# Kernel optimization log

Measured on AMD Instinct MI355X. Metric: run time of the kernel, lower is better.

Reference implementation:

```python
import jax, jax.numpy as jnp
import numpy as np

N_NODES = 50000
N_EDGES = 600000
D = 128
EDGE_VOCAB = 10


def setup_inputs() -> dict:
    key = jax.random.key(0)
    ks = jax.random.split(key, 8)
    x = jax.random.normal(ks[0], (N_NODES, D), dtype=jnp.float32)
    edge_index = jax.random.randint(ks[1], (2, N_EDGES), 0, N_NODES, dtype=jnp.int64)
    edge_weight = jax.random.randint(ks[2], (N_EDGES,), 0, EDGE_VOCAB, dtype=jnp.int64)
    cat_list = jax.random.randint(ks[3], (N_NODES,), 0, 4, dtype=jnp.int64)
    # edge embedding initialized uniform [0,1) as in torch.nn.init.uniform_
    edge_emb = jax.random.uniform(ks[4], (EDGE_VOCAB, D), dtype=jnp.float32)
    # nn.Linear default init ~ U(-1/sqrt(in), 1/sqrt(in))
    lim = 1.0 / np.sqrt(D)
    W_l = jax.random.uniform(ks[5], (D, D), minval=-lim, maxval=lim, dtype=jnp.float32)
    b_l = jax.random.uniform(ks[6], (D,), minval=-lim, maxval=lim, dtype=jnp.float32)
    W_r = jax.random.uniform(ks[7], (D, D), minval=-lim, maxval=lim, dtype=jnp.float32)
    b_r = jax.random.uniform(jax.random.fold_in(key, 99), (D,), minval=-lim, maxval=lim, dtype=jnp.float32)
    return {"x": x, "edge_emb": edge_emb, "W_l": W_l, "b_l": b_l,
            "W_r": W_r, "b_r": b_r, "edge_index": edge_index,
            "edge_weight": edge_weight, "cat_list": cat_list}


def reference(x, edge_emb, W_l, b_l, W_r, b_r, edge_index, edge_weight, cat_list):
    # Active H_GAT path: real_GNN(x, edge_index, edge_weight)
    src = edge_index[0]  # x_j (source nodes, PyG source_to_target flow)
    dst = edge_index[1]  # aggregation index
    # message: edge embedding lookup * gathered neighbor features  [E, D]
    msg = edge_emb[edge_weight] * x[src]
    # aggregate: scatter-sum to destination nodes  [N, D]
    prop = jax.ops.segment_sum(msg, dst, num_segments=x.shape[0])
    # out = lin_l(x) + lin_r(prop)
    out = x @ W_l.T + b_l + prop @ W_r.T + b_r
    return out
```

## Files before the change

kernel.cpp:

```cpp
#include <hip/hip_runtime.h>

#define N_NODES 50000
#define N_EDGES 600000
#define D 128
#define SCAN_BLOCKS ((N_NODES + 255) / 256)
#define PACK_CAP 1351680
#define PFILL_BLOCKS (PACK_CAP / 1024)
#define SENTINEL 50000u

typedef __attribute__((ext_vector_type(8))) short short8v;
typedef __attribute__((ext_vector_type(4))) float f32x4;

__device__ __forceinline__ unsigned short f2bf(float v) {
    unsigned u = __builtin_bit_cast(unsigned, v);
    u += 0x7FFFu + ((u >> 16) & 1u);
    return (unsigned short)(u >> 16);
}
__device__ __forceinline__ float bf2f(unsigned short h) {
    unsigned u = ((unsigned)h) << 16;
    return __builtin_bit_cast(float, u);
}

#define XPREP_BLOCKS ((N_NODES * D / 8 + 255) / 256)
__global__ __launch_bounds__(256) void prep_kernel(
    const float* __restrict__ Wl, const float* __restrict__ Wr,
    unsigned short* __restrict__ Bh, unsigned short* __restrict__ Bl,
    const float* __restrict__ x, unsigned short* __restrict__ xbf,
    int* __restrict__ counts, unsigned* __restrict__ packed)
{
    int bid = blockIdx.x;
    if (bid < 128) {
        int t = bid * 256 + threadIdx.x;
        int n = t >> 8;
        int k = t & 255;
        float w = (k < 128) ? Wl[n * 128 + k] : Wr[n * 128 + (k - 128)];
        unsigned short h = f2bf(w);
        Bh[t] = h;
        Bl[t] = f2bf(w - bf2f(h));
    } else if (bid < 128 + XPREP_BLOCKS) {
        int t = (bid - 128) * 256 + threadIdx.x;
        if (t < N_NODES * D / 8) {
            const float4* p = (const float4*)(x + (size_t)t * 8);
            float4 a = p[0], b = p[1];
            short8v o;
            o[0] = (short)f2bf(a.x); o[1] = (short)f2bf(a.y);
            o[2] = (short)f2bf(a.z); o[3] = (short)f2bf(a.w);
            o[4] = (short)f2bf(b.x); o[5] = (short)f2bf(b.y);
            o[6] = (short)f2bf(b.z); o[7] = (short)f2bf(b.w);
            *(short8v*)(xbf + (size_t)t * 8) = o;
        }
    } else if (bid < 128 + XPREP_BLOCKS + SCAN_BLOCKS) {
        int t = (bid - 128 - XPREP_BLOCKS) * 256 + threadIdx.x;
        if (t < N_NODES) counts[t] = 0;
    } else if (bid < 128 + XPREP_BLOCKS + SCAN_BLOCKS + PFILL_BLOCKS) {
        int t = (bid - 128 - XPREP_BLOCKS - SCAN_BLOCKS) * 1024 + threadIdx.x * 4;
        uint4 s = make_uint4(SENTINEL, SENTINEL, SENTINEL, SENTINEL);
        *(uint4*)(packed + t) = s;
    } else {
        if (threadIdx.x < 16) {
            short8v z = (short8v){0,0,0,0,0,0,0,0};
            *(short8v*)(xbf + (size_t)N_NODES * D + threadIdx.x * 8) = z;
        }
    }
}


__global__ __launch_bounds__(256) void histrank_kernel(
    const int* __restrict__ ei, int* __restrict__ counts,
    int* __restrict__ rank)
{
    int e = blockIdx.x * blockDim.x + threadIdx.x;
    if (e >= N_EDGES) return;
    rank[e] = atomicAdd(&counts[ei[N_EDGES + e]], 1);
}

__global__ __launch_bounds__(256) void scan_phase1(
    const int* __restrict__ counts, int* __restrict__ blockSums)
{
    int i = blockIdx.x * 256 + threadIdx.x;
    int v = (i < N_NODES) ? ((counts[i] + 15) & ~15) : 0;
#pragma unroll
    for (int off = 32; off > 0; off >>= 1) v += __shfl_down(v, off, 64);
    __shared__ int wsum[4];
    int lane = threadIdx.x & 63, wid = threadIdx.x >> 6;
    if (lane == 0) wsum[wid] = v;
    __syncthreads();
    if (threadIdx.x == 0)
        blockSums[blockIdx.x] = wsum[0] + wsum[1] + wsum[2] + wsum[3];
}

__global__ __launch_bounds__(256) void scan_phase2(
    const int* __restrict__ blockSums, int* __restrict__ blockOffs,
    int* __restrict__ offs)
{
    __shared__ int sh[256];
    int t = threadIdx.x;
    int v = (t < SCAN_BLOCKS) ? blockSums[t] : 0;
    sh[t] = v;
    __syncthreads();
    for (int off = 1; off < 256; off <<= 1) {
        int u = (t >= off) ? sh[t - off] : 0;
        __syncthreads();
        sh[t] += u;
        __syncthreads();
    }
    if (t < SCAN_BLOCKS) blockOffs[t] = sh[t] - v;
    if (t == 255) offs[N_NODES] = sh[255];
}

__global__ __launch_bounds__(256) void scan_phase3(
    const int* __restrict__ counts,
    const int* __restrict__ blockOffs,
    int* __restrict__ offs)
{
    int t = threadIdx.x;
    int i = blockIdx.x * 256 + t;
    int v = (i < N_NODES) ? ((counts[i] + 15) & ~15) : 0;
    int lane = t & 63, wid = t >> 6;
    int s = v;
#pragma unroll
    for (int off = 1; off < 64; off <<= 1) {
        int u = __shfl_up(s, off, 64);
        if (lane >= off) s += u;
    }
    __shared__ int wsum[4];
    if (lane == 63) wsum[wid] = s;
    __syncthreads();
    int wadd = 0;
    for (int w = 0; w < wid; w++) wadd += wsum[w];
    if (i < N_NODES)
        offs[i] = blockOffs[blockIdx.x] + s + wadd - v;
}

__global__ __launch_bounds__(256) void pack_kernel(
    const int* __restrict__ ei,
    const int* __restrict__ ew,
    const int* __restrict__ offs,
    const int* __restrict__ rank,
    unsigned* __restrict__ packed)
{
    int e = blockIdx.x * blockDim.x + threadIdx.x;
    if (e >= N_EDGES) return;
    int dst = ei[N_EDGES + e];
    int r   = rank[e];
    int pos = offs[dst] + r;
    packed[pos] = (unsigned)ei[e] | ((unsigned)ew[e] << 16);
}

__global__ __launch_bounds__(256) void aggregate_kernel(
    const unsigned short* __restrict__ xbf,
    const float* __restrict__ emb,
    const int* __restrict__ offs,
    const unsigned* __restrict__ packed,
    float* __restrict__ prop)
{
    __shared__ float emb_s[10][D];
    for (int i = threadIdx.x; i < 10 * D; i += 256)
        emb_s[i >> 7][i & 127] = emb[i];
    __syncthreads();

    int node = blockIdx.x * 8 + (threadIdx.x >> 5);
    if (node >= N_NODES) return;
    int c = (threadIdx.x & 31) * 4;

    int beg = offs[node], end = offs[node + 1];
    float4 acc = make_float4(0.f, 0.f, 0.f, 0.f);

    for (int i = beg; __any(i < end); i += 16) {
        int ib = (i < end) ? i : (PACK_CAP - 16);
        uint4 pk4[4];
#pragma unroll
        for (int qq = 0; qq < 4; qq++)
            pk4[qq] = *(const uint4*)(packed + ib + qq * 4);
        unsigned pk[16];
#pragma unroll
        for (int qq = 0; qq < 4; qq++) {
            pk[qq*4+0] = pk4[qq].x; pk[qq*4+1] = pk4[qq].y;
            pk[qq*4+2] = pk4[qq].z; pk[qq*4+3] = pk4[qq].w;
        }
        uint2 xr[16];
#pragma unroll
        for (int q = 0; q < 16; q++)
            xr[q] = *(const uint2*)(xbf + (size_t)(pk[q] & 0xFFFFu) * D + c);
#pragma unroll
        for (int q = 0; q < 16; q++) {
            float4 er = *(const float4*)&emb_s[pk[q] >> 16][c];
            acc.x += er.x * bf2f((unsigned short)(xr[q].x & 0xFFFFu));
            acc.y += er.y * bf2f((unsigned short)(xr[q].x >> 16));
            acc.z += er.z * bf2f((unsigned short)(xr[q].y & 0xFFFFu));
            acc.w += er.w * bf2f((unsigned short)(xr[q].y >> 16));
        }
    }
    *(float4*)(prop + (size_t)node * D + c) = acc;
}


__global__ void zero_kernel(float4* __restrict__ out, int n4) {
    int i = blockIdx.x * blockDim.x + threadIdx.x;
    int stride = gridDim.x * blockDim.x;
    for (; i < n4; i += stride) out[i] = make_float4(0.f, 0.f, 0.f, 0.f);
}

__global__ __launch_bounds__(256) void scatter_kernel(
    const float* __restrict__ x,
    const float* __restrict__ emb,
    const int*   __restrict__ ei,
    const int*   __restrict__ ew,
    float*       __restrict__ prop)
{
    int gid = blockIdx.x * blockDim.x + threadIdx.x;
    int e = gid >> 5;
    if (e >= N_EDGES) return;
    int d4 = (gid & 31) * 4;
    int src = ei[e];
    int dst = ei[N_EDGES + e];
    int w   = ew[e];
    float4 ev = *(const float4*)(emb + (size_t)w * D + d4);
    float4 xv = *(const float4*)(x + (size_t)src * D + d4);
    float* p = prop + (size_t)dst * D + d4;
    atomicAdd(p + 0, ev.x * xv.x);
    atomicAdd(p + 1, ev.y * xv.y);
    atomicAdd(p + 2, ev.z * xv.z);
    atomicAdd(p + 3, ev.w * xv.w);
}


__global__ __launch_bounds__(256) void mfma_gemm(
    const float* __restrict__ x,
    float*       __restrict__ out,
    const unsigned short* __restrict__ Bh,
    const unsigned short* __restrict__ Bl,
    const float* __restrict__ bl_,
    const float* __restrict__ br_)
{
    __shared__ unsigned short Ah_s[128 * 40];
    __shared__ unsigned short Al_s[128 * 40];
    __shared__ unsigned short Bh_s[128 * 40];
    __shared__ unsigned short Bl_s[128 * 40];

    const int tid  = threadIdx.x;
    const int lane = tid & 63;
    const int wave = tid >> 6;
    const int row0 = blockIdx.x * 128;

    const int wr0 = (wave >> 1) * 64;
    const int wc0 = (wave & 1) * 64;
    const int lr  = lane & 15;
    const int lk8 = (lane >> 4) * 8;

    const int srow  = tid >> 1;
    const int skoff = (tid & 1) * 16;

    f32x4 acc[4][4];
#pragma unroll
    for (int i = 0; i < 4; i++)
#pragma unroll
        for (int j = 0; j < 4; j++)
            acc[i][j] = (f32x4){0.f, 0.f, 0.f, 0.f};

    for (int kc = 0; kc < 8; ++kc) {
        const int kbase = kc * 32;
        {
            const float* Asrc = (kbase < 128) ? x : out;
            const int acol = (kbase & 127) + skoff;
            const int grow = row0 + srow;
            float v[16];
            if (grow < N_NODES) {
                const float4* p = (const float4*)(Asrc + (size_t)grow * D + acol);
#pragma unroll
                for (int q = 0; q < 4; q++) {
                    float4 f = p[q];
                    v[q*4+0] = f.x; v[q*4+1] = f.y; v[q*4+2] = f.z; v[q*4+3] = f.w;
                }
            } else {
#pragma unroll
                for (int q = 0; q < 16; q++) v[q] = 0.f;
            }
            short8v h0, h1, l0, l1;
#pragma unroll
            for (int q = 0; q < 8; q++) {
                unsigned short h = f2bf(v[q]);
                h0[q] = (short)h;
                l0[q] = (short)f2bf(v[q] - bf2f(h));
            }
#pragma unroll
            for (int q = 0; q < 8; q++) {
                unsigned short h = f2bf(v[q + 8]);
                h1[q] = (short)h;
                l1[q] = (short)f2bf(v[q + 8] - bf2f(h));
            }
            *(short8v*)(Ah_s + srow * 40 + skoff)     = h0;
            *(short8v*)(Ah_s + srow * 40 + skoff + 8) = h1;
            *(short8v*)(Al_s + srow * 40 + skoff)     = l0;
            *(short8v*)(Al_s + srow * 40 + skoff + 8) = l1;
        }
        {
            const size_t boff = (size_t)srow * 256 + kbase + skoff;
            short8v bh0 = *(const short8v*)(Bh + boff);
            short8v bh1 = *(const short8v*)(Bh + boff + 8);
            short8v bl0 = *(const short8v*)(Bl + boff);
            short8v bl1 = *(const short8v*)(Bl + boff + 8);
            *(short8v*)(Bh_s + srow * 40 + skoff)     = bh0;
            *(short8v*)(Bh_s + srow * 40 + skoff + 8) = bh1;
            *(short8v*)(Bl_s + srow * 40 + skoff)     = bl0;
            *(short8v*)(Bl_s + srow * 40 + skoff + 8) = bl1;
        }
        __syncthreads();
        short8v afh[4], afl[4];
#pragma unroll
        for (int rt = 0; rt < 4; rt++) {
            int ar = wr0 + rt * 16 + lr;
            afh[rt] = *(const short8v*)(Ah_s + ar * 40 + lk8);
            afl[rt] = *(const short8v*)(Al_s + ar * 40 + lk8);
        }
#pragma unroll
        for (int ct = 0; ct < 4; ct++) {
            int bc = wc0 + ct * 16 + lr;
            short8v bfh = *(const short8v*)(Bh_s + bc * 40 + lk8);
            short8v bfl = *(const short8v*)(Bl_s + bc * 40 + lk8);
#pragma unroll
            for (int rt = 0; rt < 4; rt++)
                acc[rt][ct] = __builtin_amdgcn_mfma_f32_16x16x32_bf16(afh[rt], bfh, acc[rt][ct], 0, 0, 0);
#pragma unroll
            for (int rt = 0; rt < 4; rt++)
                acc[rt][ct] = __builtin_amdgcn_mfma_f32_16x16x32_bf16(afl[rt], bfh, acc[rt][ct], 0, 0, 0);
#pragma unroll
            for (int rt = 0; rt < 4; rt++)
                acc[rt][ct] = __builtin_amdgcn_mfma_f32_16x16x32_bf16(afh[rt], bfl, acc[rt][ct], 0, 0, 0);
        }
        __syncthreads();
    }

    const int drow = (lane >> 4) * 4;
#pragma unroll
    for (int ct = 0; ct < 4; ct++) {
        int col = wc0 + ct * 16 + lr;
        float bias = bl_[col] + br_[col];
#pragma unroll
        for (int rt = 0; rt < 4; rt++) {
#pragma unroll
            for (int r = 0; r < 4; r++) {
                int grow = row0 + wr0 + rt * 16 + drow + r;
                if (grow < N_NODES)
                    out[(size_t)grow * D + col] = acc[rt][ct][r] + bias;
            }
        }
    }
}

extern "C" void kernel_launch(void* const* d_in, const int* in_sizes, int n_in,
                              void* d_out, int out_size, void* d_ws, size_t ws_size,
                              hipStream_t stream) {
    const float* x    = (const float*)d_in[0];
    const float* emb  = (const float*)d_in[1];
    const float* W_l  = (const float*)d_in[2];
    const float* b_l  = (const float*)d_in[3];
    const float* W_r  = (const float*)d_in[4];
    const float* b_r  = (const float*)d_in[5];
    const int*   ei   = (const int*)d_in[6];
    const int*   ew   = (const int*)d_in[7];

    float* out = (float*)d_out;

    char* wsp = (char*)d_ws;
    unsigned short* Bh  = (unsigned short*)wsp; wsp += 128 * 256 * sizeof(unsigned short);
    unsigned short* Bl  = (unsigned short*)wsp; wsp += 128 * 256 * sizeof(unsigned short);
    unsigned short* xbf = (unsigned short*)wsp; wsp += (size_t)(N_NODES + 1) * D * sizeof(unsigned short);
    int*      counts    = (int*)wsp;     wsp += N_NODES * sizeof(int);
    int*      offs      = (int*)wsp;     wsp += (N_NODES + 1) * sizeof(int);
    int*      rank      = (int*)wsp;     wsp += N_EDGES * sizeof(int);
    int*      blockSums = (int*)wsp;     wsp += SCAN_BLOCKS * sizeof(int);
    int*      blockOffs = (int*)wsp;     wsp += SCAN_BLOCKS * sizeof(int);
    unsigned* packed    = (unsigned*)wsp; wsp += (size_t)PACK_CAP * sizeof(unsigned);
    size_t needed = (size_t)(wsp - (char*)d_ws);

    if (ws_size >= needed) {
        prep_kernel<<<128 + XPREP_BLOCKS + SCAN_BLOCKS + PFILL_BLOCKS + 1, 256, 0, stream>>>(
            W_l, W_r, Bh, Bl, x, xbf, counts, packed);
        histrank_kernel<<<(N_EDGES + 255) / 256, 256, 0, stream>>>(ei, counts, rank);
        scan_phase1<<<SCAN_BLOCKS, 256, 0, stream>>>(counts, blockSums);
        scan_phase2<<<1, 256, 0, stream>>>(blockSums, blockOffs, offs);
        scan_phase3<<<SCAN_BLOCKS, 256, 0, stream>>>(counts, blockOffs, offs);
        pack_kernel<<<(N_EDGES + 255) / 256, 256, 0, stream>>>(ei, ew, offs, rank, packed);
        aggregate_kernel<<<(N_NODES + 7) / 8, 256, 0, stream>>>(xbf, emb, offs, packed, out);
        mfma_gemm<<<(N_NODES + 127) / 128, 256, 0, stream>>>(x, out, Bh, Bl, b_l, b_r);
    } else {
        prep_kernel<<<128, 256, 0, stream>>>(W_l, W_r, Bh, Bl, x, xbf, counts, packed);
        int n4 = N_NODES * D / 4;
        zero_kernel<<<(n4 + 255) / 256, 256, 0, stream>>>((float4*)out, n4);
        long long work = (long long)N_EDGES * 32;
        scatter_kernel<<<(int)((work + 255) / 256), 256, 0, stream>>>(x, emb, ei, ew, out);
        mfma_gemm<<<(N_NODES + 127) / 128, 256, 0, stream>>>(x, out, Bh, Bl, b_l, b_r);
    }
}
```

Baseline: 106.7 us.

## Pre-split x and prop into bf16 hi/lo, shrink CSR padding, merge scan phases

```diff
diff --git a/kernel.cpp b/kernel.cpp
--- a/kernel.cpp
+++ b/kernel.cpp
@@ -4,7 +4,8 @@
 #define N_EDGES 600000
 #define D 128
 #define SCAN_BLOCKS ((N_NODES + 255) / 256)
-#define PACK_CAP 1351680
+#define PAD 8
+#define PACK_CAP 950272
 #define PFILL_BLOCKS (PACK_CAP / 1024)
 #define SENTINEL 50000u
 
@@ -25,7 +26,8 @@
 __global__ __launch_bounds__(256) void prep_kernel(
     const float* __restrict__ Wl, const float* __restrict__ Wr,
     unsigned short* __restrict__ Bh, unsigned short* __restrict__ Bl,
-    const float* __restrict__ x, unsigned short* __restrict__ xbf,
+    const float* __restrict__ x,
+    unsigned short* __restrict__ xh, unsigned short* __restrict__ xl,
     int* __restrict__ counts, unsigned* __restrict__ packed)
 {
     int bid = blockIdx.x;
@@ -42,12 +44,16 @@
         if (t < N_NODES * D / 8) {
             const float4* p = (const float4*)(x + (size_t)t * 8);
             float4 a = p[0], b = p[1];
-            short8v o;
-            o[0] = (short)f2bf(a.x); o[1] = (short)f2bf(a.y);
-            o[2] = (short)f2bf(a.z); o[3] = (short)f2bf(a.w);
-            o[4] = (short)f2bf(b.x); o[5] = (short)f2bf(b.y);
-            o[6] = (short)f2bf(b.z); o[7] = (short)f2bf(b.w);
-            *(short8v*)(xbf + (size_t)t * 8) = o;
+            float v[8] = {a.x, a.y, a.z, a.w, b.x, b.y, b.z, b.w};
+            short8v oh, ol;
+#pragma unroll
+            for (int q = 0; q < 8; q++) {
+                unsigned short h = f2bf(v[q]);
+                oh[q] = (short)h;
+                ol[q] = (short)f2bf(v[q] - bf2f(h));
+            }
+            *(short8v*)(xh + (size_t)t * 8) = oh;
+            *(short8v*)(xl + (size_t)t * 8) = ol;
         }
     } else if (bid < 128 + XPREP_BLOCKS + SCAN_BLOCKS) {
         int t = (bid - 128 - XPREP_BLOCKS) * 256 + threadIdx.x;
@@ -59,7 +65,7 @@
     } else {
         if (threadIdx.x < 16) {
             short8v z = (short8v){0,0,0,0,0,0,0,0};
-            *(short8v*)(xbf + (size_t)N_NODES * D + threadIdx.x * 8) = z;
+            *(short8v*)(xh + (size_t)N_NODES * D + threadIdx.x * 8) = z;
         }
     }
 }
@@ -78,7 +84,7 @@
     const int* __restrict__ counts, int* __restrict__ blockSums)
 {
     int i = blockIdx.x * 256 + threadIdx.x;
-    int v = (i < N_NODES) ? ((counts[i] + 15) & ~15) : 0;
+    int v = (i < N_NODES) ? ((counts[i] + PAD - 1) & ~(PAD - 1)) : 0;
 #pragma unroll
     for (int off = 32; off > 0; off >>= 1) v += __shfl_down(v, off, 64);
     __shared__ int wsum[4];
@@ -89,14 +95,15 @@
         blockSums[blockIdx.x] = wsum[0] + wsum[1] + wsum[2] + wsum[3];
 }
 
-__global__ __launch_bounds__(256) void scan_phase2(
-    const int* __restrict__ blockSums, int* __restrict__ blockOffs,
+__global__ __launch_bounds__(256) void scan_phase23(
+    const int* __restrict__ counts,
+    const int* __restrict__ blockSums,
     int* __restrict__ offs)
 {
     __shared__ int sh[256];
     int t = threadIdx.x;
-    int v = (t < SCAN_BLOCKS) ? blockSums[t] : 0;
-    sh[t] = v;
+    int bs = (t < SCAN_BLOCKS) ? blockSums[t] : 0;
+    sh[t] = bs;
     __syncthreads();
     for (int off = 1; off < 256; off <<= 1) {
         int u = (t >= off) ? sh[t - off] : 0;
@@ -104,18 +111,11 @@
         sh[t] += u;
         __syncthreads();
     }
-    if (t < SCAN_BLOCKS) blockOffs[t] = sh[t] - v;
-    if (t == 255) offs[N_NODES] = sh[255];
-}
-
-__global__ __launch_bounds__(256) void scan_phase3(
-    const int* __restrict__ counts,
-    const int* __restrict__ blockOffs,
-    int* __restrict__ offs)
-{
-    int t = threadIdx.x;
+    int blockOff = (blockIdx.x > 0) ? sh[blockIdx.x - 1] : 0;
+    if (blockIdx.x == 0 && t == 0) offs[N_NODES] = sh[SCAN_BLOCKS - 1];
+
     int i = blockIdx.x * 256 + t;
-    int v = (i < N_NODES) ? ((counts[i] + 15) & ~15) : 0;
+    int v = (i < N_NODES) ? ((counts[i] + PAD - 1) & ~(PAD - 1)) : 0;
     int lane = t & 63, wid = t >> 6;
     int s = v;
 #pragma unroll
@@ -129,7 +129,7 @@
     int wadd = 0;
     for (int w = 0; w < wid; w++) wadd += wsum[w];
     if (i < N_NODES)
-        offs[i] = blockOffs[blockIdx.x] + s + wadd - v;
+        offs[i] = blockOff + s + wadd - v;
 }
 
 __global__ __launch_bounds__(256) void pack_kernel(
@@ -148,11 +148,11 @@
 }
 
 __global__ __launch_bounds__(256) void aggregate_kernel(
-    const unsigned short* __restrict__ xbf,
+    const unsigned short* __restrict__ xh,
     const float* __restrict__ emb,
     const int* __restrict__ offs,
     const unsigned* __restrict__ packed,
-    float* __restrict__ prop)
+    unsigned short* __restrict__ ph, unsigned short* __restrict__ pl)
 {
     __shared__ float emb_s[10][D];
     for (int i = threadIdx.x; i < 10 * D; i += 256)
@@ -166,24 +166,17 @@
     int beg = offs[node], end = offs[node + 1];
     float4 acc = make_float4(0.f, 0.f, 0.f, 0.f);
 
-    for (int i = beg; __any(i < end); i += 16) {
-        int ib = (i < end) ? i : (PACK_CAP - 16);
-        uint4 pk4[4];
-#pragma unroll
-        for (int qq = 0; qq < 4; qq++)
-            pk4[qq] = *(const uint4*)(packed + ib + qq * 4);
-        unsigned pk[16];
-#pragma unroll
-        for (int qq = 0; qq < 4; qq++) {
-            pk[qq*4+0] = pk4[qq].x; pk[qq*4+1] = pk4[qq].y;
-            pk[qq*4+2] = pk4[qq].z; pk[qq*4+3] = pk4[qq].w;
-        }
-        uint2 xr[16];
-#pragma unroll
-        for (int q = 0; q < 16; q++)
-            xr[q] = *(const uint2*)(xbf + (size_t)(pk[q] & 0xFFFFu) * D + c);
-#pragma unroll
-        for (int q = 0; q < 16; q++) {
+    for (int i = beg; __any(i < end); i += PAD) {
+        int ib = (i < end) ? i : (PACK_CAP - PAD);
+        uint4 a0 = *(const uint4*)(packed + ib);
+        uint4 a1 = *(const uint4*)(packed + ib + 4);
+        unsigned pk[8] = {a0.x, a0.y, a0.z, a0.w, a1.x, a1.y, a1.z, a1.w};
+        uint2 xr[8];
+#pragma unroll
+        for (int q = 0; q < 8; q++)
+            xr[q] = *(const uint2*)(xh + (size_t)(pk[q] & 0xFFFFu) * D + c);
+#pragma unroll
+        for (int q = 0; q < 8; q++) {
             float4 er = *(const float4*)&emb_s[pk[q] >> 16][c];
             acc.x += er.x * bf2f((unsigned short)(xr[q].x & 0xFFFFu));
             acc.y += er.y * bf2f((unsigned short)(xr[q].x >> 16));
@@ -191,7 +184,127 @@
             acc.w += er.w * bf2f((unsigned short)(xr[q].y >> 16));
         }
     }
-    *(float4*)(prop + (size_t)node * D + c) = acc;
+    float v[4] = {acc.x, acc.y, acc.z, acc.w};
+    unsigned short h[4], l[4];
+#pragma unroll
+    for (int q = 0; q < 4; q++) {
+        h[q] = f2bf(v[q]);
+        l[q] = f2bf(v[q] - bf2f(h[q]));
+    }
+    unsigned h01 = (unsigned)h[0] | ((unsigned)h[1] << 16);
+    unsigned h23 = (unsigned)h[2] | ((unsigned)h[3] << 16);
+    unsigned l01 = (unsigned)l[0] | ((unsigned)l[1] << 16);
+    unsigned l23 = (unsigned)l[2] | ((unsigned)l[3] << 16);
+    *(uint2*)(ph + (size_t)node * D + c) = make_uint2(h01, h23);
+    *(uint2*)(pl + (size_t)node * D + c) = make_uint2(l01, l23);
+}
+
+__global__ __launch_bounds__(256) void mfma_gemm(
+    const unsigned short* __restrict__ xh, const unsigned short* __restrict__ xl,
+    const unsigned short* __restrict__ ph, const unsigned short* __restrict__ pl,
+    float*       __restrict__ out,
+    const unsigned short* __restrict__ Bh,
+    const unsigned short* __restrict__ Bl,
+    const float* __restrict__ bl_,
+    const float* __restrict__ br_)
+{
+    __shared__ unsigned short Ah_s[128 * 40];
+    __shared__ unsigned short Al_s[128 * 40];
+    __shared__ unsigned short Bh_s[128 * 40];
+    __shared__ unsigned short Bl_s[128 * 40];
+
+    const int tid  = threadIdx.x;
+    const int lane = tid & 63;
+    const int wave = tid >> 6;
+    const int row0 = blockIdx.x * 128;
+
+    const int wr0 = (wave >> 1) * 64;
+    const int wc0 = (wave & 1) * 64;
+    const int lr  = lane & 15;
+    const int lk8 = (lane >> 4) * 8;
+
+    const int srow  = tid >> 1;
+    const int skoff = (tid & 1) * 16;
+
+    f32x4 acc[4][4];
+#pragma unroll
+    for (int i = 0; i < 4; i++)
+#pragma unroll
+        for (int j = 0; j < 4; j++)
+            acc[i][j] = (f32x4){0.f, 0.f, 0.f, 0.f};
+
+    for (int kc = 0; kc < 8; ++kc) {
+        const int kbase = kc * 32;
+        {
+            const unsigned short* sH = (kbase < 128) ? xh : ph;
+            const unsigned short* sL = (kbase < 128) ? xl : pl;
+            const size_t off = (size_t)(row0 + srow) * D + (kbase & 127) + skoff;
+            short8v h0, h1, l0, l1;
+            if (row0 + srow < N_NODES) {
+                h0 = *(const short8v*)(sH + off);
+                h1 = *(const short8v*)(sH + off + 8);
+                l0 = *(const short8v*)(sL + off);
+                l1 = *(const short8v*)(sL + off + 8);
+            } else {
+                h0 = h1 = l0 = l1 = (short8v){0,0,0,0,0,0,0,0};
+            }
+            *(short8v*)(Ah_s + srow * 40 + skoff)     = h0;
+            *(short8v*)(Ah_s + srow * 40 + skoff + 8) = h1;
+            *(short8v*)(Al_s + srow * 40 + skoff)     = l0;
+            *(short8v*)(Al_s + srow * 40 + skoff + 8) = l1;
+        }
+        {
+            const size_t boff = (size_t)srow * 256 + kbase + skoff;
+            short8v bh0 = *(const short8v*)(Bh + boff);
+            short8v bh1 = *(const short8v*)(Bh + boff + 8);
+            short8v bl0 = *(const short8v*)(Bl + boff);
+            short8v bl1 = *(const short8v*)(Bl + boff + 8);
+            *(short8v*)(Bh_s + srow * 40 + skoff)     = bh0;
+            *(short8v*)(Bh_s + srow * 40 + skoff + 8) = bh1;
+            *(short8v*)(Bl_s + srow * 40 + skoff)     = bl0;
+            *(short8v*)(Bl_s + srow * 40 + skoff + 8) = bl1;
+        }
+        __syncthreads();
+        short8v afh[4], afl[4];
+#pragma unroll
+        for (int rt = 0; rt < 4; rt++) {
+            int ar = wr0 + rt * 16 + lr;
+            afh[rt] = *(const short8v*)(Ah_s + ar * 40 + lk8);
+            afl[rt] = *(const short8v*)(Al_s + ar * 40 + lk8);
+        }
+#pragma unroll
+        for (int ct = 0; ct < 4; ct++) {
+            int bc = wc0 + ct * 16 + lr;
+            short8v bfh = *(const short8v*)(Bh_s + bc * 40 + lk8);
+            short8v bfl = *(const short8v*)(Bl_s + bc * 40 + lk8);
+#pragma unroll
+            for (int rt = 0; rt < 4; rt++)
+                acc[rt][ct] = __builtin_amdgcn_mfma_f32_16x16x32_bf16(afh[rt], bfh, acc[rt][ct], 0, 0, 0);
+#pragma unroll
+            for (int rt = 0; rt < 4; rt++)
+                acc[rt][ct] = __builtin_amdgcn_mfma_f32_16x16x32_bf16(afl[rt], bfh, acc[rt][ct], 0, 0, 0);
+#pragma unroll
+            for (int rt = 0; rt < 4; rt++)
+                acc[rt][ct] = __builtin_amdgcn_mfma_f32_16x16x32_bf16(afh[rt], bfl, acc[rt][ct], 0, 0, 0);
+        }
+        __syncthreads();
+    }
+
+    const int drow = (lane >> 4) * 4;
+#pragma unroll
+    for (int ct = 0; ct < 4; ct++) {
+        int col = wc0 + ct * 16 + lr;
+        float bias = bl_[col] + br_[col];
+#pragma unroll
+        for (int rt = 0; rt < 4; rt++) {
+#pragma unroll
+            for (int r = 0; r < 4; r++) {
+                int grow = row0 + wr0 + rt * 16 + drow + r;
+                if (grow < N_NODES)
+                    out[(size_t)grow * D + col] = acc[rt][ct][r] + bias;
+            }
+        }
+    }
 }
 
 
@@ -224,8 +337,7 @@
     atomicAdd(p + 3, ev.w * xv.w);
 }
 
-
-__global__ __launch_bounds__(256) void mfma_gemm(
+__global__ __launch_bounds__(256) void mfma_gemm_fb(
     const float* __restrict__ x,
     float*       __restrict__ out,
     const unsigned short* __restrict__ Bh,
@@ -242,12 +354,10 @@
     const int lane = tid & 63;
     const int wave = tid >> 6;
     const int row0 = blockIdx.x * 128;
-
     const int wr0 = (wave >> 1) * 64;
     const int wc0 = (wave & 1) * 64;
     const int lr  = lane & 15;
     const int lk8 = (lane >> 4) * 8;
-
     const int srow  = tid >> 1;
     const int skoff = (tid & 1) * 16;
 
@@ -296,14 +406,10 @@
         }
         {
             const size_t boff = (size_t)srow * 256 + kbase + skoff;
-            short8v bh0 = *(const short8v*)(Bh + boff);
-            short8v bh1 = *(const short8v*)(Bh + boff + 8);
-            short8v bl0 = *(const short8v*)(Bl + boff);
-            short8v bl1 = *(const short8v*)(Bl + boff + 8);
-            *(short8v*)(Bh_s + srow * 40 + skoff)     = bh0;
-            *(short8v*)(Bh_s + srow * 40 + skoff + 8) = bh1;
-            *(short8v*)(Bl_s + srow * 40 + skoff)     = bl0;
-            *(short8v*)(Bl_s + srow * 40 + skoff + 8) = bl1;
+            *(short8v*)(Bh_s + srow * 40 + skoff)     = *(const short8v*)(Bh + boff);
+            *(short8v*)(Bh_s + srow * 40 + skoff + 8) = *(const short8v*)(Bh + boff + 8);
+            *(short8v*)(Bl_s + srow * 40 + skoff)     = *(const short8v*)(Bl + boff);
+            *(short8v*)(Bl_s + srow * 40 + skoff + 8) = *(const short8v*)(Bl + boff + 8);
         }
         __syncthreads();
         short8v afh[4], afl[4];
@@ -365,31 +471,32 @@
     char* wsp = (char*)d_ws;
     unsigned short* Bh  = (unsigned short*)wsp; wsp += 128 * 256 * sizeof(unsigned short);
     unsigned short* Bl  = (unsigned short*)wsp; wsp += 128 * 256 * sizeof(unsigned short);
-    unsigned short* xbf = (unsigned short*)wsp; wsp += (size_t)(N_NODES + 1) * D * sizeof(unsigned short);
+    unsigned short* xh  = (unsigned short*)wsp; wsp += (size_t)(N_NODES + 1) * D * sizeof(unsigned short);
+    unsigned short* xl  = (unsigned short*)wsp; wsp += (size_t)N_NODES * D * sizeof(unsigned short);
+    unsigned short* ph  = (unsigned short*)wsp; wsp += (size_t)N_NODES * D * sizeof(unsigned short);
+    unsigned short* pl  = (unsigned short*)wsp; wsp += (size_t)N_NODES * D * sizeof(unsigned short);
     int*      counts    = (int*)wsp;     wsp += N_NODES * sizeof(int);
     int*      offs      = (int*)wsp;     wsp += (N_NODES + 1) * sizeof(int);
     int*      rank      = (int*)wsp;     wsp += N_EDGES * sizeof(int);
     int*      blockSums = (int*)wsp;     wsp += SCAN_BLOCKS * sizeof(int);
-    int*      blockOffs = (int*)wsp;     wsp += SCAN_BLOCKS * sizeof(int);
     unsigned* packed    = (unsigned*)wsp; wsp += (size_t)PACK_CAP * sizeof(unsigned);
     size_t needed = (size_t)(wsp - (char*)d_ws);
 
     if (ws_size >= needed) {
         prep_kernel<<<128 + XPREP_BLOCKS + SCAN_BLOCKS + PFILL_BLOCKS + 1, 256, 0, stream>>>(
-            W_l, W_r, Bh, Bl, x, xbf, counts, packed);
+            W_l, W_r, Bh, Bl, x, xh, xl, counts, packed);
         histrank_kernel<<<(N_EDGES + 255) / 256, 256, 0, stream>>>(ei, counts, rank);
         scan_phase1<<<SCAN_BLOCKS, 256, 0, stream>>>(counts, blockSums);
-        scan_phase2<<<1, 256, 0, stream>>>(blockSums, blockOffs, offs);
-        scan_phase3<<<SCAN_BLOCKS, 256, 0, stream>>>(counts, blockOffs, offs);
+        scan_phase23<<<SCAN_BLOCKS, 256, 0, stream>>>(counts, blockSums, offs);
         pack_kernel<<<(N_EDGES + 255) / 256, 256, 0, stream>>>(ei, ew, offs, rank, packed);
-        aggregate_kernel<<<(N_NODES + 7) / 8, 256, 0, stream>>>(xbf, emb, offs, packed, out);
-        mfma_gemm<<<(N_NODES + 127) / 128, 256, 0, stream>>>(x, out, Bh, Bl, b_l, b_r);
+        aggregate_kernel<<<(N_NODES + 7) / 8, 256, 0, stream>>>(xh, emb, offs, packed, ph, pl);
+        mfma_gemm<<<(N_NODES + 127) / 128, 256, 0, stream>>>(xh, xl, ph, pl, out, Bh, Bl, b_l, b_r);
     } else {
-        prep_kernel<<<128, 256, 0, stream>>>(W_l, W_r, Bh, Bl, x, xbf, counts, packed);
+        prep_kernel<<<128, 256, 0, stream>>>(W_l, W_r, Bh, Bl, x, xh, xl, counts, packed);
         int n4 = N_NODES * D / 4;
         zero_kernel<<<(n4 + 255) / 256, 256, 0, stream>>>((float4*)out, n4);
         long long work = (long long)N_EDGES * 32;
         scatter_kernel<<<(int)((work + 255) / 256), 256, 0, stream>>>(x, emb, ei, ew, out);
-        mfma_gemm<<<(N_NODES + 127) / 128, 256, 0, stream>>>(x, out, Bh, Bl, b_l, b_r);
-    }
-}
+        mfma_gemm_fb<<<(N_NODES + 127) / 128, 256, 0, stream>>>(x, out, Bh, Bl, b_l, b_r);
+    }
+}
```

Result: no change. 106.4 us (-0.2%).
